# Optimization experiments

Hardware: AMD Instinct MI355X
Metric: run time of the kernel (lower is better)

## Reference

```python
import jax, jax.numpy as jnp
import numpy as np

BANDWIDTH = 8.0  # gaussian kernel std


def setup_inputs() -> dict:
    key = jax.random.key(0)
    k1, k2 = jax.random.split(key)
    B, N, M, D = 2, 8192, 8192, 64
    return {
        "points": jax.random.normal(k1, (B, N, D), dtype=jnp.float32),
        "ref_points": jax.random.normal(k2, (B, M, D), dtype=jnp.float32),
    }


def reference(points, ref_points):
    # Squared pairwise distances via the |x|^2 + |y|^2 - 2<x,y> expansion
    # (same math as ((x_i - y_j)**2).sum(-1), avoids a [B,N,M,D] intermediate).
    sq_p = jnp.sum(points * points, axis=-1)          # [B,N]
    sq_r = jnp.sum(ref_points * ref_points, axis=-1)  # [B,M]
    s_ij = (sq_p[:, :, None] + sq_r[:, None, :]
            - 2.0 * jnp.einsum('bnd,bmd->bnm', points, ref_points))  # [B,N,M]
    # Gaussian kernel
    k_ij = jnp.exp(s_ij * (-1.0 / (2.0 * BANDWIDTH ** 2)))  # [B,N,M]
    # Weighted mean of reference points (nominator.sum(2) / k_ij.sum(2))
    nominator = jnp.einsum('bnm,bmd->bnd', k_ij, ref_points)  # [B,N,D]
    denominator = jnp.sum(k_ij, axis=-1, keepdims=True)       # [B,N,1]
    return nominator / denominator
```

## Files before the change

### kernel.cpp

```cpp
#include <hip/hip_runtime.h>

constexpr int B_ = 2, N_ = 8192, M_ = 8192, Dd = 64;
constexpr int TN = 128;
constexpr int TM = 128;
constexpr int SPLIT = 8;
constexpr int MCHUNK = M_ / SPLIT;
constexpr int NCHUNKS = MCHUNK / TM;
constexpr int NT = N_ / TN;
constexpr float LOG2E   = 1.4426950408889634f;
constexpr float SCALE_S = LOG2E / 64.0f;
constexpr float SCALE_N = -LOG2E / 128.0f;

using s16x8 = __attribute__((ext_vector_type(8))) short;
using f32x4 = __attribute__((ext_vector_type(4))) float;

#if defined(__has_builtin)
#if __has_builtin(__builtin_amdgcn_exp2f)
#define EXP2(x) __builtin_amdgcn_exp2f(x)
#endif
#endif
#ifndef EXP2
#define EXP2(x) exp2f(x)
#endif

__device__ __forceinline__ unsigned short f2bf(float f) {
  unsigned u = __builtin_bit_cast(unsigned, f);
  u += 0x7FFFu + ((u >> 16) & 1u);
  return (unsigned short)(u >> 16);
}

__device__ __forceinline__ f32x4 mfma16(s16x8 a, s16x8 b, f32x4 c) {
  return __builtin_amdgcn_mfma_f32_16x16x32_bf16(a, b, c, 0, 0, 0);
}


__global__ __launch_bounds__(256, 2) void msflash_kernel(
    const float* __restrict__ pts, const float* __restrict__ ref,
    float* __restrict__ num_acc, float* __restrict__ den_acc) {
  __shared__ unsigned short ldsY [TM][72];
  __shared__ unsigned short ldsYT[Dd][136];
  __shared__ unsigned short ldsP [4][32][72];
  __shared__ float lds_an2[TN];
  __shared__ float lds_bm2[TM];

  const int tid  = threadIdx.x;
  const int w    = tid >> 6;
  const int lane = tid & 63;
  const int l15  = lane & 15, quad = lane >> 4;

  const int s  = blockIdx.x & (SPLIT - 1);
  const int r  = blockIdx.x >> 3;
  const int bb = r / NT;
  const int nt = r % NT;
  const int n0 = nt * TN;
  const int m_begin = s * MCHUNK;

  unsigned short (*ldsX)[72] = (unsigned short (*)[72]) & ldsP[0][0][0];
  {
    const int rowl = tid >> 1, half = tid & 1;
    const float* gp = pts + ((size_t)bb * N_ + n0 + rowl) * Dd + half * 32;
    float4 f[8];
#pragma unroll
    for (int i = 0; i < 8; i++) f[i] = ((const float4*)gp)[i];
    float sq = 0.f;
#pragma unroll
    for (int i = 0; i < 8; i++)
      sq += f[i].x * f[i].x + f[i].y * f[i].y + f[i].z * f[i].z + f[i].w * f[i].w;
    sq += __shfl_xor(sq, 1);
    if (half == 0) lds_an2[rowl] = sq * SCALE_N;
    unsigned short hv[32];
#pragma unroll
    for (int i = 0; i < 8; i++) {
      hv[4 * i + 0] = f2bf(f[i].x); hv[4 * i + 1] = f2bf(f[i].y);
      hv[4 * i + 2] = f2bf(f[i].z); hv[4 * i + 3] = f2bf(f[i].w);
    }
    uint4* dv = (uint4*)&ldsX[rowl][half * 32];
#pragma unroll
    for (int i = 0; i < 4; i++) {
      dv[i] = make_uint4(
        (unsigned)hv[8*i+0] | ((unsigned)hv[8*i+1] << 16),
        (unsigned)hv[8*i+2] | ((unsigned)hv[8*i+3] << 16),
        (unsigned)hv[8*i+4] | ((unsigned)hv[8*i+5] << 16),
        (unsigned)hv[8*i+6] | ((unsigned)hv[8*i+7] << 16));
    }
  }
  __syncthreads();

  s16x8 ax[2][2];
  f32x4 anr[2];
#pragma unroll
  for (int rt = 0; rt < 2; rt++) {
#pragma unroll
    for (int ks = 0; ks < 2; ks++)
      ax[rt][ks] = *(const s16x8*)&ldsX[w * 32 + rt * 16 + l15][ks * 32 + quad * 8];
    anr[rt] = *(const f32x4*)&lds_an2[w * 32 + rt * 16 + quad * 4];
  }

  f32x4 o[2][4], den[2];
#pragma unroll
  for (int rt = 0; rt < 2; rt++) {
    den[rt] = f32x4{0.f, 0.f, 0.f, 0.f};
#pragma unroll
    for (int dt = 0; dt < 4; dt++) o[rt][dt] = f32x4{0.f, 0.f, 0.f, 0.f};
  }
  s16x8 ones;
#pragma unroll
  for (int j = 0; j < 8; j++) ones[j] = (l15 == 0) ? (short)0x3F80 : (short)0;

  for (int c = 0; c < NCHUNKS; c++) {
    __syncthreads();
    {
      const int rowl = tid >> 1, half = tid & 1;
      const int mg = m_begin + c * TM + rowl;
      const float* gp = ref + ((size_t)bb * M_ + mg) * Dd + half * 32;
      float4 f[8];
#pragma unroll
      for (int i = 0; i < 8; i++) f[i] = ((const float4*)gp)[i];
      float sq = 0.f;
#pragma unroll
      for (int i = 0; i < 8; i++)
        sq += f[i].x * f[i].x + f[i].y * f[i].y + f[i].z * f[i].z + f[i].w * f[i].w;
      sq += __shfl_xor(sq, 1);
      if (half == 0) lds_bm2[rowl] = sq * SCALE_N;
      unsigned short hv[32];
#pragma unroll
      for (int i = 0; i < 8; i++) {
        hv[4 * i + 0] = f2bf(f[i].x); hv[4 * i + 1] = f2bf(f[i].y);
        hv[4 * i + 2] = f2bf(f[i].z); hv[4 * i + 3] = f2bf(f[i].w);
      }
      uint4* dv = (uint4*)&ldsY[rowl][half * 32];
#pragma unroll
      for (int i = 0; i < 4; i++) {
        dv[i] = make_uint4(
          (unsigned)hv[8*i+0] | ((unsigned)hv[8*i+1] << 16),
          (unsigned)hv[8*i+2] | ((unsigned)hv[8*i+3] << 16),
          (unsigned)hv[8*i+4] | ((unsigned)hv[8*i+5] << 16),
          (unsigned)hv[8*i+6] | ((unsigned)hv[8*i+7] << 16));
      }
#pragma unroll
      for (int j = 0; j < 32; j++) ldsYT[half * 32 + j][rowl] = hv[j];
    }
    __syncthreads();

#pragma unroll
    for (int h = 0; h < 2; h++) {
      f32x4 sf[2][4];
#pragma unroll
      for (int ct = 0; ct < 4; ct++) {
        s16x8 by0 = *(const s16x8*)&ldsY[h * 64 + ct * 16 + l15][quad * 8];
        s16x8 by1 = *(const s16x8*)&ldsY[h * 64 + ct * 16 + l15][32 + quad * 8];
#pragma unroll
        for (int rt = 0; rt < 2; rt++) {
          f32x4 acc = f32x4{0.f, 0.f, 0.f, 0.f};
          acc = mfma16(ax[rt][0], by0, acc);
          acc = mfma16(ax[rt][1], by1, acc);
          sf[rt][ct] = acc;
        }
      }
#pragma unroll
      for (int ct = 0; ct < 4; ct++) {
        float bm2v = lds_bm2[h * 64 + ct * 16 + l15];
#pragma unroll
        for (int rt = 0; rt < 2; rt++) {
          unsigned short* pb = &ldsP[w][rt * 16 + quad * 4][ct * 16 + l15];
#pragma unroll
          for (int g = 0; g < 4; g++) {
            float arg = sf[rt][ct][g] * SCALE_S + anr[rt][g] + bm2v;
            pb[(size_t)g * 72] = f2bf(EXP2(arg));
          }
        }
      }
      s16x8 pf[2][2];
#pragma unroll
      for (int rt = 0; rt < 2; rt++)
#pragma unroll
        for (int ks = 0; ks < 2; ks++)
          pf[rt][ks] = *(const s16x8*)&ldsP[w][rt * 16 + l15][ks * 32 + quad * 8];
#pragma unroll
      for (int dt = 0; dt < 4; dt++) {
        s16x8 bv0 = *(const s16x8*)&ldsYT[dt * 16 + l15][h * 64 + quad * 8];
        s16x8 bv1 = *(const s16x8*)&ldsYT[dt * 16 + l15][h * 64 + 32 + quad * 8];
#pragma unroll
        for (int rt = 0; rt < 2; rt++) {
          o[rt][dt] = mfma16(pf[rt][0], bv0, o[rt][dt]);
          o[rt][dt] = mfma16(pf[rt][1], bv1, o[rt][dt]);
        }
      }
#pragma unroll
      for (int rt = 0; rt < 2; rt++) {
        den[rt] = mfma16(pf[rt][0], ones, den[rt]);
        den[rt] = mfma16(pf[rt][1], ones, den[rt]);
      }
    }
  }

  float* nb = num_acc + ((size_t)bb * N_ + n0) * Dd;
#pragma unroll
  for (int rt = 0; rt < 2; rt++) {
    const int row0 = w * 32 + rt * 16 + quad * 4;
#pragma unroll
    for (int dt = 0; dt < 4; dt++) {
      const int col = dt * 16 + l15;
#pragma unroll
      for (int g = 0; g < 4; g++)
        atomicAdd(&nb[(size_t)(row0 + g) * Dd + col], o[rt][dt][g]);
    }
    if (l15 == 0) {
#pragma unroll
      for (int g = 0; g < 4; g++)
        atomicAdd(&den_acc[(size_t)bb * N_ + n0 + row0 + g], den[rt][g]);
    }
  }
}

__global__ __launch_bounds__(256) void msdiv_kernel(
    const float* __restrict__ num, const float* __restrict__ den,
    float* __restrict__ out) {
  const int i = blockIdx.x * 256 + threadIdx.x;
  float4 v = ((const float4*)num)[i];
  const float inv = 1.0f / den[i >> 4];
  ((float4*)out)[i] = make_float4(v.x * inv, v.y * inv, v.z * inv, v.w * inv);
}

extern "C" void kernel_launch(void* const* d_in, const int* in_sizes, int n_in,
                              void* d_out, int out_size, void* d_ws, size_t ws_size,
                              hipStream_t stream) {
  const float* pts = (const float*)d_in[0];
  const float* ref = (const float*)d_in[1];
  float* out = (float*)d_out;
  float* num = (float*)d_ws;
  float* den = num + (size_t)B_ * N_ * Dd;
  const size_t acc_bytes = ((size_t)B_ * N_ * Dd + (size_t)B_ * N_) * sizeof(float);

  hipMemsetAsync(d_ws, 0, acc_bytes, stream);
  msflash_kernel<<<dim3(B_ * NT * SPLIT), dim3(256), 0, stream>>>(pts, ref, num, den);
  const int tot4 = B_ * N_ * Dd / 4;
  msdiv_kernel<<<dim3(tot4 / 256), dim3(256), 0, stream>>>(num, den, out);
}
```

Baseline: 157.7 us.

## Halve M tile, swap MFMA operand roles, and pack bf16 LDS writes

Shrinks the reference tile from 128 to 64 rows, which cuts LDS use (ldsY and ldsYT become smaller) and raises the launch-bounds occupancy target from 2 to 4 blocks per CU. The MFMA operands are swapped so the score and accumulator fragments come out transposed. This lets each lane write packed 4-element bf16 P values to LDS in one store instead of four scalar shorts. Conversion and squared-norm work is fused into the global load loop using paired bf16 packing. The trade-off is twice as many chunk iterations with their barriers, and tighter register pressure under the higher occupancy bound.

Result: slower. 233.9 us (+48.3%).

```diff
diff --git a/kernel.cpp b/kernel.cpp
--- a/kernel.cpp
+++ b/kernel.cpp
@@ -2,7 +2,7 @@
 
 constexpr int B_ = 2, N_ = 8192, M_ = 8192, Dd = 64;
 constexpr int TN = 128;
-constexpr int TM = 128;
+constexpr int TM = 64;
 constexpr int SPLIT = 8;
 constexpr int MCHUNK = M_ / SPLIT;
 constexpr int NCHUNKS = MCHUNK / TM;
@@ -28,17 +28,19 @@
   u += 0x7FFFu + ((u >> 16) & 1u);
   return (unsigned short)(u >> 16);
 }
-
+__device__ __forceinline__ unsigned pk2(float lo, float hi) {
+  return (unsigned)f2bf(lo) | ((unsigned)f2bf(hi) << 16);
+}
 __device__ __forceinline__ f32x4 mfma16(s16x8 a, s16x8 b, f32x4 c) {
   return __builtin_amdgcn_mfma_f32_16x16x32_bf16(a, b, c, 0, 0, 0);
 }
 
 
-__global__ __launch_bounds__(256, 2) void msflash_kernel(
+__global__ __launch_bounds__(256, 4) void msflash_kernel(
     const float* __restrict__ pts, const float* __restrict__ ref,
     float* __restrict__ num_acc, float* __restrict__ den_acc) {
   __shared__ unsigned short ldsY [TM][72];
-  __shared__ unsigned short ldsYT[Dd][136];
+  __shared__ unsigned short ldsYT[Dd][72];
   __shared__ unsigned short ldsP [4][32][72];
   __shared__ float lds_an2[TN];
   __shared__ float lds_bm2[TM];
@@ -59,41 +61,32 @@
   {
     const int rowl = tid >> 1, half = tid & 1;
     const float* gp = pts + ((size_t)bb * N_ + n0 + rowl) * Dd + half * 32;
-    float4 f[8];
-#pragma unroll
-    for (int i = 0; i < 8; i++) f[i] = ((const float4*)gp)[i];
     float sq = 0.f;
-#pragma unroll
-    for (int i = 0; i < 8; i++)
-      sq += f[i].x * f[i].x + f[i].y * f[i].y + f[i].z * f[i].z + f[i].w * f[i].w;
+    unsigned pkd[16];
+#pragma unroll
+    for (int i = 0; i < 8; i++) {
+      float4 f = ((const float4*)gp)[i];
+      sq += f.x * f.x + f.y * f.y + f.z * f.z + f.w * f.w;
+      pkd[2 * i + 0] = pk2(f.x, f.y);
+      pkd[2 * i + 1] = pk2(f.z, f.w);
+    }
     sq += __shfl_xor(sq, 1);
     if (half == 0) lds_an2[rowl] = sq * SCALE_N;
-    unsigned short hv[32];
-#pragma unroll
-    for (int i = 0; i < 8; i++) {
-      hv[4 * i + 0] = f2bf(f[i].x); hv[4 * i + 1] = f2bf(f[i].y);
-      hv[4 * i + 2] = f2bf(f[i].z); hv[4 * i + 3] = f2bf(f[i].w);
-    }
     uint4* dv = (uint4*)&ldsX[rowl][half * 32];
 #pragma unroll
-    for (int i = 0; i < 4; i++) {
-      dv[i] = make_uint4(
-        (unsigned)hv[8*i+0] | ((unsigned)hv[8*i+1] << 16),
-        (unsigned)hv[8*i+2] | ((unsigned)hv[8*i+3] << 16),
-        (unsigned)hv[8*i+4] | ((unsigned)hv[8*i+5] << 16),
-        (unsigned)hv[8*i+6] | ((unsigned)hv[8*i+7] << 16));
-    }
+    for (int i = 0; i < 4; i++)
+      dv[i] = make_uint4(pkd[4 * i], pkd[4 * i + 1], pkd[4 * i + 2], pkd[4 * i + 3]);
   }
   __syncthreads();
 
-  s16x8 ax[2][2];
-  f32x4 anr[2];
+  s16x8 bx[2][2];
+  float anr_s[2];
 #pragma unroll
   for (int rt = 0; rt < 2; rt++) {
 #pragma unroll
     for (int ks = 0; ks < 2; ks++)
-      ax[rt][ks] = *(const s16x8*)&ldsX[w * 32 + rt * 16 + l15][ks * 32 + quad * 8];
-    anr[rt] = *(const f32x4*)&lds_an2[w * 32 + rt * 16 + quad * 4];
+      bx[rt][ks] = *(const s16x8*)&ldsX[w * 32 + rt * 16 + l15][ks * 32 + quad * 8];
+    anr_s[rt] = lds_an2[w * 32 + rt * 16 + l15];
   }
 
   f32x4 o[2][4], den[2];
@@ -110,106 +103,93 @@
   for (int c = 0; c < NCHUNKS; c++) {
     __syncthreads();
     {
-      const int rowl = tid >> 1, half = tid & 1;
-      const int mg = m_begin + c * TM + rowl;
-      const float* gp = ref + ((size_t)bb * M_ + mg) * Dd + half * 32;
-      float4 f[8];
-#pragma unroll
-      for (int i = 0; i < 8; i++) f[i] = ((const float4*)gp)[i];
+      const int rowl = tid >> 2, q = tid & 3;
+      const float* gp = ref + ((size_t)bb * M_ + m_begin + c * TM + rowl) * Dd + q * 16;
       float sq = 0.f;
-#pragma unroll
-      for (int i = 0; i < 8; i++)
-        sq += f[i].x * f[i].x + f[i].y * f[i].y + f[i].z * f[i].z + f[i].w * f[i].w;
+      unsigned pkd[8];
+#pragma unroll
+      for (int i = 0; i < 4; i++) {
+        float4 f = ((const float4*)gp)[i];
+        sq += f.x * f.x + f.y * f.y + f.z * f.z + f.w * f.w;
+        pkd[2 * i + 0] = pk2(f.x, f.y);
+        pkd[2 * i + 1] = pk2(f.z, f.w);
+      }
       sq += __shfl_xor(sq, 1);
-      if (half == 0) lds_bm2[rowl] = sq * SCALE_N;
-      unsigned short hv[32];
-#pragma unroll
-      for (int i = 0; i < 8; i++) {
-        hv[4 * i + 0] = f2bf(f[i].x); hv[4 * i + 1] = f2bf(f[i].y);
-        hv[4 * i + 2] = f2bf(f[i].z); hv[4 * i + 3] = f2bf(f[i].w);
-      }
-      uint4* dv = (uint4*)&ldsY[rowl][half * 32];
-#pragma unroll
-      for (int i = 0; i < 4; i++) {
-        dv[i] = make_uint4(
-          (unsigned)hv[8*i+0] | ((unsigned)hv[8*i+1] << 16),
-          (unsigned)hv[8*i+2] | ((unsigned)hv[8*i+3] << 16),
-          (unsigned)hv[8*i+4] | ((unsigned)hv[8*i+5] << 16),
-          (unsigned)hv[8*i+6] | ((unsigned)hv[8*i+7] << 16));
-      }
-#pragma unroll
-      for (int j = 0; j < 32; j++) ldsYT[half * 32 + j][rowl] = hv[j];
+      sq += __shfl_xor(sq, 2);
+      if (q == 0) lds_bm2[rowl] = sq * SCALE_N;
+      uint4* dv = (uint4*)&ldsY[rowl][q * 16];
+      dv[0] = make_uint4(pkd[0], pkd[1], pkd[2], pkd[3]);
+      dv[1] = make_uint4(pkd[4], pkd[5], pkd[6], pkd[7]);
+#pragma unroll
+      for (int j = 0; j < 8; j++) {
+        ldsYT[q * 16 + 2 * j + 0][rowl] = (unsigned short)pkd[j];
+        ldsYT[q * 16 + 2 * j + 1][rowl] = (unsigned short)(pkd[j] >> 16);
+      }
     }
     __syncthreads();
 
-#pragma unroll
-    for (int h = 0; h < 2; h++) {
-      f32x4 sf[2][4];
-#pragma unroll
-      for (int ct = 0; ct < 4; ct++) {
-        s16x8 by0 = *(const s16x8*)&ldsY[h * 64 + ct * 16 + l15][quad * 8];
-        s16x8 by1 = *(const s16x8*)&ldsY[h * 64 + ct * 16 + l15][32 + quad * 8];
-#pragma unroll
-        for (int rt = 0; rt < 2; rt++) {
-          f32x4 acc = f32x4{0.f, 0.f, 0.f, 0.f};
-          acc = mfma16(ax[rt][0], by0, acc);
-          acc = mfma16(ax[rt][1], by1, acc);
-          sf[rt][ct] = acc;
-        }
-      }
-#pragma unroll
-      for (int ct = 0; ct < 4; ct++) {
-        float bm2v = lds_bm2[h * 64 + ct * 16 + l15];
-#pragma unroll
-        for (int rt = 0; rt < 2; rt++) {
-          unsigned short* pb = &ldsP[w][rt * 16 + quad * 4][ct * 16 + l15];
-#pragma unroll
-          for (int g = 0; g < 4; g++) {
-            float arg = sf[rt][ct][g] * SCALE_S + anr[rt][g] + bm2v;
-            pb[(size_t)g * 72] = f2bf(EXP2(arg));
-          }
-        }
-      }
-      s16x8 pf[2][2];
-#pragma unroll
-      for (int rt = 0; rt < 2; rt++)
-#pragma unroll
-        for (int ks = 0; ks < 2; ks++)
-          pf[rt][ks] = *(const s16x8*)&ldsP[w][rt * 16 + l15][ks * 32 + quad * 8];
-#pragma unroll
-      for (int dt = 0; dt < 4; dt++) {
-        s16x8 bv0 = *(const s16x8*)&ldsYT[dt * 16 + l15][h * 64 + quad * 8];
-        s16x8 bv1 = *(const s16x8*)&ldsYT[dt * 16 + l15][h * 64 + 32 + quad * 8];
-#pragma unroll
-        for (int rt = 0; rt < 2; rt++) {
-          o[rt][dt] = mfma16(pf[rt][0], bv0, o[rt][dt]);
-          o[rt][dt] = mfma16(pf[rt][1], bv1, o[rt][dt]);
-        }
-      }
+    f32x4 sf[2][4];
+#pragma unroll
+    for (int ct = 0; ct < 4; ct++) {
+      s16x8 a0 = *(const s16x8*)&ldsY[ct * 16 + l15][quad * 8];
+      s16x8 a1 = *(const s16x8*)&ldsY[ct * 16 + l15][32 + quad * 8];
 #pragma unroll
       for (int rt = 0; rt < 2; rt++) {
-        den[rt] = mfma16(pf[rt][0], ones, den[rt]);
-        den[rt] = mfma16(pf[rt][1], ones, den[rt]);
-      }
+        f32x4 acc = f32x4{0.f, 0.f, 0.f, 0.f};
+        acc = mfma16(a0, bx[rt][0], acc);
+        acc = mfma16(a1, bx[rt][1], acc);
+        sf[rt][ct] = acc;
+      }
+    }
+#pragma unroll
+    for (int ct = 0; ct < 4; ct++) {
+      f32x4 bm = *(const f32x4*)&lds_bm2[ct * 16 + quad * 4];
+#pragma unroll
+      for (int rt = 0; rt < 2; rt++) {
+        float e0 = EXP2(sf[rt][ct][0] * SCALE_S + (anr_s[rt] + bm[0]));
+        float e1 = EXP2(sf[rt][ct][1] * SCALE_S + (anr_s[rt] + bm[1]));
+        float e2 = EXP2(sf[rt][ct][2] * SCALE_S + (anr_s[rt] + bm[2]));
+        float e3 = EXP2(sf[rt][ct][3] * SCALE_S + (anr_s[rt] + bm[3]));
+        uint2 w2 = make_uint2(pk2(e0, e1), pk2(e2, e3));
+        *(uint2*)&ldsP[w][rt * 16 + l15][ct * 16 + quad * 4] = w2;
+      }
+    }
+    s16x8 pf[2][2];
+#pragma unroll
+    for (int rt = 0; rt < 2; rt++)
+#pragma unroll
+      for (int ks = 0; ks < 2; ks++)
+        pf[rt][ks] = *(const s16x8*)&ldsP[w][rt * 16 + l15][ks * 32 + quad * 8];
+#pragma unroll
+    for (int dt = 0; dt < 4; dt++) {
+      s16x8 a0 = *(const s16x8*)&ldsYT[dt * 16 + l15][quad * 8];
+      s16x8 a1 = *(const s16x8*)&ldsYT[dt * 16 + l15][32 + quad * 8];
+#pragma unroll
+      for (int rt = 0; rt < 2; rt++) {
+        o[rt][dt] = mfma16(a0, pf[rt][0], o[rt][dt]);
+        o[rt][dt] = mfma16(a1, pf[rt][1], o[rt][dt]);
+      }
+    }
+#pragma unroll
+    for (int rt = 0; rt < 2; rt++) {
+      den[rt] = mfma16(ones, pf[rt][0], den[rt]);
+      den[rt] = mfma16(ones, pf[rt][1], den[rt]);
     }
   }
 
   float* nb = num_acc + ((size_t)bb * N_ + n0) * Dd;
 #pragma unroll
   for (int rt = 0; rt < 2; rt++) {
-    const int row0 = w * 32 + rt * 16 + quad * 4;
+    const int nrow = w * 32 + rt * 16 + l15;
 #pragma unroll
     for (int dt = 0; dt < 4; dt++) {
-      const int col = dt * 16 + l15;
+      const int d0 = dt * 16 + quad * 4;
 #pragma unroll
       for (int g = 0; g < 4; g++)
-        atomicAdd(&nb[(size_t)(row0 + g) * Dd + col], o[rt][dt][g]);
-    }
-    if (l15 == 0) {
-#pragma unroll
-      for (int g = 0; g < 4; g++)
-        atomicAdd(&den_acc[(size_t)bb * N_ + n0 + row0 + g], den[rt][g]);
-    }
+        atomicAdd(&nb[(size_t)nrow * Dd + d0 + g], o[rt][dt][g]);
+    }
+    if (quad == 0)
+      atomicAdd(&den_acc[(size_t)bb * N_ + n0 + nrow], den[rt][0]);
   }
 }
 
```
